# Optimization experiments

Hardware: AMD Instinct MI355X
Metric: run time of the kernel (lower is better)

## Reference

```python
import jax, jax.numpy as jnp
import numpy as np

N_Q, N_K = 4096, 32768
D_IN_Q, D_IN_V = 1024, 1024
D_QK, D_V = 512, 512
MASK_VAL = -1000.0


def setup_inputs() -> dict:
    key = jax.random.key(0)
    ks = jax.random.split(key, 9)
    X1 = jax.random.normal(ks[0], (N_Q, D_IN_Q), dtype=jnp.float32)
    X2 = jax.random.normal(ks[1], (N_K, D_IN_V), dtype=jnp.float32)
    row_map = jax.random.randint(ks[2], (N_K,), 0, N_Q, dtype=jnp.int32)
    # Linear params (stored as (in, out) for x @ W + b), xavier-ish scale
    def lin(k, din, dout):
        s = jnp.sqrt(6.0 / (din + dout)).astype(jnp.float32)
        return jax.random.uniform(k, (din, dout), jnp.float32, -s, s)
    Wq = lin(ks[3], D_IN_Q, D_QK); bq = jnp.zeros((D_QK,), jnp.float32)
    Wk = lin(ks[4], D_IN_V, D_QK); bk = jnp.zeros((D_QK,), jnp.float32)
    Wv = lin(ks[5], D_IN_V, D_V); bv = jnp.zeros((D_V,), jnp.float32)
    return {"X1": X1, "X2": X2, "Wq": Wq, "bq": bq, "Wk": Wk, "bk": bk,
            "Wv": Wv, "bv": bv, "row_map": row_map}


def reference(X1, X2, Wq, bq, Wk, bk, Wv, bv, row_map):
    n_q = X1.shape[0]
    n_k = X2.shape[0]
    Q = X1 @ Wq + bq                      # (n_q, d_qk)
    K = X2 @ Wk + bk                      # (n_k, d_qk)
    V = X2 @ Wv + bv                      # (n_k, d_v)
    scale = 1.0 / jnp.sqrt(jnp.float32(Q.shape[1]))
    S = (Q @ K.T) * scale                 # (n_q, n_k)
    cols = jnp.arange(n_k)
    # Keep only entries (row_map[j], j); everything else set to -1000 (as in torch)
    S_masked = jnp.full_like(S, MASK_VAL).at[row_map, cols].set(S[row_map, cols])
    W = jax.nn.softmax(S_masked, axis=1)  # (n_q, n_k)
    C = W @ V                             # (n_q, d_v)
    # Queries with no related keys get zero rows (torch skips them entirely)
    counts = jax.ops.segment_sum(jnp.ones((n_k,), jnp.float32), row_map,
                                 num_segments=n_q)
    return jnp.where(counts[:, None] > 0, C, jnp.zeros_like(C))
```

## Files before the change

kernel.cpp:

```cpp
#include <hip/hip_runtime.h>

typedef unsigned short bhalf;
typedef __bf16 bf16x8 __attribute__((ext_vector_type(8)));
typedef float f32x4 __attribute__((ext_vector_type(4)));

#define NQ 4096
#define NK 32768
#define DIN 1024
#define DQK 512
#define SCALE 0.044194173824159216f

__device__ __forceinline__ bhalf f2bf(float f) {
  union { float f; unsigned u; } c; c.f = f;
  unsigned u = c.u;
  return (bhalf)((u + 0x7fffu + ((u >> 16) & 1u)) >> 16);
}

__global__ void cvt_kernel(const float* __restrict__ in, bhalf* __restrict__ out, int n4) {
  const int i = blockIdx.x * 256 + threadIdx.x;
  float4 v = ((const float4*)in)[i];
  uint2 o;
  o.x = (unsigned)f2bf(v.x) | ((unsigned)f2bf(v.y) << 16);
  o.y = (unsigned)f2bf(v.z) | ((unsigned)f2bf(v.w) << 16);
  ((uint2*)out)[i] = o;
}

__global__ __launch_bounds__(256) void transpose_cvt_kernel(
    const float* __restrict__ in, bhalf* __restrict__ out) {
  const int Kdim = 1024, Ndim = 512;
  __shared__ float tile[32][33];
  const int tx = threadIdx.x, ty = threadIdx.y;
  const int x = blockIdx.x * 32 + tx;
#pragma unroll
  for (int yy = 0; yy < 32; yy += 8) {
    const int y = blockIdx.y * 32 + ty + yy;
    tile[ty + yy][tx] = in[(size_t)y * Ndim + x];
  }
  __syncthreads();
  const int k = blockIdx.y * 32 + tx;
#pragma unroll
  for (int yy = 0; yy < 32; yy += 8) {
    const int n = blockIdx.x * 32 + ty + yy;
    out[(size_t)n * Kdim + k] = f2bf(tile[tx][ty + yy]);
  }
}

__global__ __launch_bounds__(256) void gh_kernel(
    const float* __restrict__ Wk, const float* __restrict__ Wq,
    const float* __restrict__ bq, const float* __restrict__ bk,
    float* __restrict__ g_s, float* __restrict__ h, float* __restrict__ scal) {
  const int w = blockIdx.x * 4 + (threadIdx.x >> 6);
  const int lane = threadIdx.x & 63;
  if (w >= 2049) return;
  const float* row; const float* vec;
  if (w < 1024)      { row = Wk + (size_t)w * 512; vec = bq; }
  else if (w < 2048) { row = Wq + (size_t)(w - 1024) * 512; vec = bk; }
  else               { row = bq; vec = bk; }
  float s = 0.f;
#pragma unroll
  for (int t = 0; t < 2; t++) {
    float4 a = *(const float4*)(row + t * 256 + lane * 4);
    float4 b = *(const float4*)(vec + t * 256 + lane * 4);
    s += a.x * b.x + a.y * b.y + a.z * b.z + a.w * b.w;
  }
#pragma unroll
  for (int d = 32; d; d >>= 1) s += __shfl_xor(s, d);
  if (lane == 0) {
    if (w < 1024) g_s[w] = s * SCALE;
    else if (w < 2048) h[w - 1024] = s;
    else scal[0] = s;
  }
}

__global__ __launch_bounds__(256) void e_kernel(
    const float* __restrict__ X1, const float* __restrict__ h,
    const float* __restrict__ scal, float* __restrict__ ebuf) {
  const int i = blockIdx.x * 4 + (threadIdx.x >> 6);
  const int lane = threadIdx.x & 63;
  const float* xr = X1 + (size_t)i * 1024;
  float s = 0.f;
#pragma unroll
  for (int t = 0; t < 4; t++) {
    float4 a = *(const float4*)(xr + t * 256 + lane * 4);
    float4 b = *(const float4*)(h + t * 256 + lane * 4);
    s += a.x * b.x + a.y * b.y + a.z * b.z + a.w * b.w;
  }
#pragma unroll
  for (int d = 32; d; d >>= 1) s += __shfl_xor(s, d);
  if (lane == 0) ebuf[i] = (s + scal[0]) * SCALE;
}

template <int MODE>
__global__ __launch_bounds__(256) void gemm_core(
    const bhalf* __restrict__ A, const bhalf* __restrict__ Bt,
    const float* __restrict__ bias, const int* __restrict__ cnt,
    void* __restrict__ Cout, int M, int N, int K, int nnt) {
  __shared__ __align__(16) bhalf As[128 * 64];
  __shared__ __align__(16) bhalf Bs[128 * 64];
  const int bid = blockIdx.x;
  const int mt = bid / nnt, nt = bid % nnt;
  const int bmb = mt * 128, bnb = nt * 128;

  const int tid = threadIdx.x;
  const int lane = tid & 63;
  const int wv = tid >> 6;
  const int wm = (wv & 1) * 64;
  const int wn = (wv >> 1) * 64;
  const int quad = lane >> 4;
  const int l15 = lane & 15;

  f32x4 acc[4][4];
#pragma unroll
  for (int i = 0; i < 4; i++)
#pragma unroll
    for (int j = 0; j < 4; j++)
#pragma unroll
      for (int r = 0; r < 4; r++) acc[i][j][r] = 0.0f;

  const int srow = lane >> 3;
  const int scol = (lane & 7) ^ srow;

  for (int kb = 0; kb < K; kb += 64) {
#pragma unroll
    for (int r = 0; r < 4; r++) {
      const int chunk = wv * 4 + r;
      const int row = chunk * 8 + srow;
      const size_t goff = (size_t)kb + (size_t)scol * 8;
      __builtin_amdgcn_global_load_lds(
          (__attribute__((address_space(1))) unsigned int*)(A + (size_t)(bmb + row) * K + goff),
          (__attribute__((address_space(3))) unsigned int*)(As + chunk * 512), 16, 0, 0);
      __builtin_amdgcn_global_load_lds(
          (__attribute__((address_space(1))) unsigned int*)(Bt + (size_t)(bnb + row) * K + goff),
          (__attribute__((address_space(3))) unsigned int*)(Bs + chunk * 512), 16, 0, 0);
    }
    __syncthreads();
#pragma unroll
    for (int ks = 0; ks < 2; ks++) {
      const int su = ((ks * 4 + quad) ^ (lane & 7)) * 8;
      bf16x8 af[4], bfr[4];
#pragma unroll
      for (int i = 0; i < 4; i++) {
        af[i]  = *(const bf16x8*)(As + (wm + i * 16 + l15) * 64 + su);
        bfr[i] = *(const bf16x8*)(Bs + (wn + i * 16 + l15) * 64 + su);
      }
#pragma unroll
      for (int i = 0; i < 4; i++)
#pragma unroll
        for (int j = 0; j < 4; j++)
          acc[i][j] = __builtin_amdgcn_mfma_f32_16x16x32_bf16(af[i], bfr[j], acc[i][j], 0, 0, 0);
    }
    __syncthreads();
  }
#pragma unroll
  for (int j = 0; j < 4; j++) {
    const int col = bnb + wn + j * 16 + l15;
    const float bs = (MODE >= 1) ? bias[col] : 0.0f;
#pragma unroll
    for (int i = 0; i < 4; i++) {
#pragma unroll
      for (int r = 0; r < 4; r++) {
        const int row = bmb + wm + i * 16 + quad * 4 + r;
        const float v = acc[i][j][r];
        if (MODE == 0) {
          ((bhalf*)Cout)[(size_t)row * N + col] = f2bf(v * SCALE);
        } else if (MODE == 1) {
          ((float*)Cout)[(size_t)row * N + col] = v + bs;
        } else {
          ((float*)Cout)[(size_t)row * N + col] = (cnt[row] > 0) ? (v + bs) : 0.0f;
        }
      }
    }
  }
}

__global__ void hist_kernel(const int* __restrict__ rm, int* __restrict__ cnt) {
  const int j = blockIdx.x * 256 + threadIdx.x;
  atomicAdd(&cnt[rm[j]], 1);
}

__global__ __launch_bounds__(1024) void scan_kernel(const int* __restrict__ cnt,
                                                    int* __restrict__ off,
                                                    int* __restrict__ cur) {
  const int t = threadIdx.x;
  int4 v = ((const int4*)cnt)[t];
  const int sum = v.x + v.y + v.z + v.w;
  const int lane = t & 63, w = t >> 6;
  int x = sum;
#pragma unroll
  for (int d = 1; d < 64; d <<= 1) {
    int y = __shfl_up(x, d);
    if (lane >= d) x += y;
  }
  __shared__ int wsum[16];
  if (lane == 63) wsum[w] = x;
  __syncthreads();
  if (t == 0) {
    int a = 0;
    for (int i = 0; i < 16; i++) { int tv = wsum[i]; wsum[i] = a; a += tv; }
  }
  __syncthreads();
  const int excl = x - sum + wsum[w];
  int4 o; o.x = excl; o.y = o.x + v.x; o.z = o.y + v.y; o.w = o.z + v.z;
  ((int4*)off)[t] = o;
  ((int4*)cur)[t] = o;
}

__global__ void scatter_kernel(const int* __restrict__ rm, int* __restrict__ cur,
                               int* __restrict__ keylist) {
  const int j = blockIdx.x * 256 + threadIdx.x;
  const int p = atomicAdd(&cur[rm[j]], 1);
  keylist[p] = j;
}

__global__ __launch_bounds__(256) void scorewsum_kernel(
    const float* __restrict__ P, const float* __restrict__ X2,
    const float* __restrict__ ebuf, const int* __restrict__ off,
    const int* __restrict__ cnt, const int* __restrict__ keylist,
    bhalf* __restrict__ Ub) {
  __shared__ float wbuf[4][256];
  const int wv = threadIdx.x >> 6;
  const int i = blockIdx.x * 4 + wv;
  const int lane = threadIdx.x & 63;
  const int c = cnt[i], base = off[i];
  const float* Prow = P + (size_t)i * 1024;
  float4 p[4];
#pragma unroll
  for (int t = 0; t < 4; t++) p[t] = *(const float4*)(Prow + t * 256 + lane * 4);
  const float e_i = ebuf[i];
  float sumw = 0.f;
  for (int pp = 0; pp < c; pp++) {
    const int j = keylist[base + pp];
    const float* xr = X2 + (size_t)j * 1024;
    float s = 0.f;
#pragma unroll
    for (int t = 0; t < 4; t++) {
      float4 x = *(const float4*)(xr + t * 256 + lane * 4);
      s += p[t].x * x.x + p[t].y * x.y + p[t].z * x.z + p[t].w * x.w;
    }
#pragma unroll
    for (int d = 32; d; d >>= 1) s += __shfl_xor(s, d);
    const float w = __expf(s + e_i);
    sumw += w;
    if (lane == 0) wbuf[wv][pp] = w;
  }
  __syncthreads();
  float4 u[4] = {};
  for (int pp = 0; pp < c; pp++) {
    const int j = keylist[base + pp];
    const float w = wbuf[wv][pp];
    const float* xr = X2 + (size_t)j * 1024;
#pragma unroll
    for (int t = 0; t < 4; t++) {
      float4 x = *(const float4*)(xr + t * 256 + lane * 4);
      u[t].x += w * x.x; u[t].y += w * x.y; u[t].z += w * x.z; u[t].w += w * x.w;
    }
  }
  const float inv = (c > 0) ? 1.f / sumw : 0.f;
  bhalf* urow = Ub + (size_t)i * 1024;
#pragma unroll
  for (int t = 0; t < 4; t++) {
    uint2 o;
    o.x = (unsigned)f2bf(u[t].x * inv) | ((unsigned)f2bf(u[t].y * inv) << 16);
    o.y = (unsigned)f2bf(u[t].z * inv) | ((unsigned)f2bf(u[t].w * inv) << 16);
    *(uint2*)(urow + t * 256 + lane * 4) = o;
  }
}

extern "C" void kernel_launch(void* const* d_in, const int* in_sizes, int n_in,
                              void* d_out, int out_size, void* d_ws, size_t ws_size,
                              hipStream_t stream) {
  const float* X1 = (const float*)d_in[0];
  const float* X2 = (const float*)d_in[1];
  const float* Wq = (const float*)d_in[2];
  const float* bq = (const float*)d_in[3];
  const float* Wk = (const float*)d_in[4];
  const float* bk = (const float*)d_in[5];
  const float* Wv = (const float*)d_in[6];
  const float* bv = (const float*)d_in[7];
  const int* row_map = (const int*)d_in[8];
  float* out = (float*)d_out;

  char* p = (char*)d_ws;
  bhalf* X1b  = (bhalf*)p; p += (size_t)NQ * DIN * 2;
  bhalf* Wq_b = (bhalf*)p; p += (size_t)DIN * DQK * 2;
  bhalf* Wk_b = (bhalf*)p; p += (size_t)DIN * DQK * 2;
  bhalf* WvT  = (bhalf*)p; p += (size_t)DQK * DIN * 2;
  bhalf* Bt2  = (bhalf*)p; p += (size_t)DIN * DIN * 2;
  float* Pbuf = (float*)p; p += (size_t)NQ * DIN * 4;
  bhalf* Ub   = (bhalf*)p; p += (size_t)NQ * DIN * 2;
  float* g_s  = (float*)p; p += DIN * 4;
  float* h    = (float*)p; p += DIN * 4;
  float* ebuf = (float*)p; p += NQ * 4;
  float* scal = (float*)p; p += 256;
  int* cnt    = (int*)p;   p += NQ * 4;
  int* off    = (int*)p;   p += NQ * 4;
  int* cur    = (int*)p;   p += NQ * 4;
  int* keylist = (int*)p;  p += NK * 4;

  hipMemsetAsync(cnt, 0, (size_t)NQ * 4, stream);

  cvt_kernel<<<NQ * DIN / 4 / 256, 256, 0, stream>>>(X1, X1b, NQ * DIN / 4);
  cvt_kernel<<<DIN * DQK / 4 / 256, 256, 0, stream>>>(Wq, Wq_b, DIN * DQK / 4);
  cvt_kernel<<<DIN * DQK / 4 / 256, 256, 0, stream>>>(Wk, Wk_b, DIN * DQK / 4);
  transpose_cvt_kernel<<<dim3(16, 32), dim3(32, 8), 0, stream>>>(Wv, WvT);
  gh_kernel<<<513, 256, 0, stream>>>(Wk, Wq, bq, bk, g_s, h, scal);
  e_kernel<<<NQ / 4, 256, 0, stream>>>(X1, h, scal, ebuf);

  hist_kernel<<<NK / 256, 256, 0, stream>>>(row_map, cnt);
  scan_kernel<<<1, 1024, 0, stream>>>(cnt, off, cur);
  scatter_kernel<<<NK / 256, 256, 0, stream>>>(row_map, cur, keylist);

  gemm_core<0><<<64, 256, 0, stream>>>(Wk_b, Wq_b, nullptr, nullptr, Bt2, 1024, 1024, 512, 8);
  gemm_core<1><<<256, 256, 0, stream>>>(X1b, Bt2, g_s, nullptr, Pbuf, 4096, 1024, 1024, 8);

  scorewsum_kernel<<<NQ / 4, 256, 0, stream>>>(Pbuf, X2, ebuf, off, cnt, keylist, Ub);

  gemm_core<2><<<128, 256, 0, stream>>>(Ub, WvT, bv, cnt, out, 4096, 512, 1024, 4);
}
```

Measured before the change: 324.7 us.

## Fuse prep kernels, single-pass score/weighted-sum, and smaller M tiles for small GEMMs

Merges the three cvt launches, the Wv transpose, the gh reduction and the histogram into one block-indexed prep kernel to cut launch overhead. Moves the per-query e_i computation into the score kernel and merges its two passes over X2 into one. Each X2 row is now read once into registers and used for both the score and the weighted sum, removing the shared buffer and the barrier. Adds an MI template parameter so the Bt2 and output GEMMs use 64-row tiles and launch twice as many blocks, trading per-block reuse for better CU coverage.

```diff
diff --git a/kernel.cpp b/kernel.cpp
--- a/kernel.cpp
+++ b/kernel.cpp
@@ -10,108 +10,96 @@
 #define DQK 512
 #define SCALE 0.044194173824159216f
 
-__device__ __forceinline__ bhalf f2bf(float f) {
+__device__ __forceinline__ unsigned f2bf(float f) {
   union { float f; unsigned u; } c; c.f = f;
   unsigned u = c.u;
-  return (bhalf)((u + 0x7fffu + ((u >> 16) & 1u)) >> 16);
-}
-
-__global__ void cvt_kernel(const float* __restrict__ in, bhalf* __restrict__ out, int n4) {
-  const int i = blockIdx.x * 256 + threadIdx.x;
-  float4 v = ((const float4*)in)[i];
-  uint2 o;
-  o.x = (unsigned)f2bf(v.x) | ((unsigned)f2bf(v.y) << 16);
-  o.y = (unsigned)f2bf(v.z) | ((unsigned)f2bf(v.w) << 16);
-  ((uint2*)out)[i] = o;
-}
-
-__global__ __launch_bounds__(256) void transpose_cvt_kernel(
-    const float* __restrict__ in, bhalf* __restrict__ out) {
-  const int Kdim = 1024, Ndim = 512;
+  return (u + 0x7fffu + ((u >> 16) & 1u)) >> 16;
+}
+
+__global__ __launch_bounds__(256) void prep_kernel(
+    const float* __restrict__ X1, const float* __restrict__ Wq,
+    const float* __restrict__ Wk, const float* __restrict__ Wv,
+    const float* __restrict__ bq, const float* __restrict__ bk,
+    const int* __restrict__ rm,
+    bhalf* __restrict__ X1b, bhalf* __restrict__ Wq_b, bhalf* __restrict__ Wk_b,
+    bhalf* __restrict__ WvT, float* __restrict__ g_s, float* __restrict__ h,
+    float* __restrict__ scal, int* __restrict__ cnt) {
   __shared__ float tile[32][33];
-  const int tx = threadIdx.x, ty = threadIdx.y;
-  const int x = blockIdx.x * 32 + tx;
-#pragma unroll
-  for (int yy = 0; yy < 32; yy += 8) {
-    const int y = blockIdx.y * 32 + ty + yy;
-    tile[ty + yy][tx] = in[(size_t)y * Ndim + x];
-  }
-  __syncthreads();
-  const int k = blockIdx.y * 32 + tx;
-#pragma unroll
-  for (int yy = 0; yy < 32; yy += 8) {
-    const int n = blockIdx.x * 32 + ty + yy;
-    out[(size_t)n * Kdim + k] = f2bf(tile[tx][ty + yy]);
-  }
-}
-
-__global__ __launch_bounds__(256) void gh_kernel(
-    const float* __restrict__ Wk, const float* __restrict__ Wq,
-    const float* __restrict__ bq, const float* __restrict__ bk,
-    float* __restrict__ g_s, float* __restrict__ h, float* __restrict__ scal) {
-  const int w = blockIdx.x * 4 + (threadIdx.x >> 6);
-  const int lane = threadIdx.x & 63;
-  if (w >= 2049) return;
-  const float* row; const float* vec;
-  if (w < 1024)      { row = Wk + (size_t)w * 512; vec = bq; }
-  else if (w < 2048) { row = Wq + (size_t)(w - 1024) * 512; vec = bk; }
-  else               { row = bq; vec = bk; }
-  float s = 0.f;
-#pragma unroll
-  for (int t = 0; t < 2; t++) {
-    float4 a = *(const float4*)(row + t * 256 + lane * 4);
-    float4 b = *(const float4*)(vec + t * 256 + lane * 4);
-    s += a.x * b.x + a.y * b.y + a.z * b.z + a.w * b.w;
-  }
-#pragma unroll
-  for (int d = 32; d; d >>= 1) s += __shfl_xor(s, d);
-  if (lane == 0) {
-    if (w < 1024) g_s[w] = s * SCALE;
-    else if (w < 2048) h[w - 1024] = s;
-    else scal[0] = s;
-  }
-}
-
-__global__ __launch_bounds__(256) void e_kernel(
-    const float* __restrict__ X1, const float* __restrict__ h,
-    const float* __restrict__ scal, float* __restrict__ ebuf) {
-  const int i = blockIdx.x * 4 + (threadIdx.x >> 6);
-  const int lane = threadIdx.x & 63;
-  const float* xr = X1 + (size_t)i * 1024;
-  float s = 0.f;
-#pragma unroll
-  for (int t = 0; t < 4; t++) {
-    float4 a = *(const float4*)(xr + t * 256 + lane * 4);
-    float4 b = *(const float4*)(h + t * 256 + lane * 4);
-    s += a.x * b.x + a.y * b.y + a.z * b.z + a.w * b.w;
-  }
-#pragma unroll
-  for (int d = 32; d; d >>= 1) s += __shfl_xor(s, d);
-  if (lane == 0) ebuf[i] = (s + scal[0]) * SCALE;
-}
-
-template <int MODE>
+  const int b = blockIdx.x;
+  const int tid = threadIdx.x;
+  if (b < 5120) {
+    const float* in; bhalf* out; int idx;
+    if (b < 4096)      { in = X1; out = X1b; idx = b * 256 + tid; }
+    else if (b < 4608) { in = Wq; out = Wq_b; idx = (b - 4096) * 256 + tid; }
+    else               { in = Wk; out = Wk_b; idx = (b - 4608) * 256 + tid; }
+    float4 v = ((const float4*)in)[idx];
+    uint2 o;
+    o.x = f2bf(v.x) | (f2bf(v.y) << 16);
+    o.y = f2bf(v.z) | (f2bf(v.w) << 16);
+    ((uint2*)out)[idx] = o;
+  } else if (b < 5632) {
+    const int bb = b - 5120;
+    const int bx = bb & 15, by = bb >> 4;
+    const int tx = tid & 31, ty = tid >> 5;
+    const int x = bx * 32 + tx;
+#pragma unroll
+    for (int yy = 0; yy < 32; yy += 8)
+      tile[ty + yy][tx] = Wv[(size_t)(by * 32 + ty + yy) * 512 + x];
+    __syncthreads();
+    const int k = by * 32 + tx;
+#pragma unroll
+    for (int yy = 0; yy < 32; yy += 8)
+      WvT[(size_t)(bx * 32 + ty + yy) * 1024 + k] = (bhalf)f2bf(tile[tx][ty + yy]);
+  } else if (b < 6145) {
+    const int w = (b - 5632) * 4 + (tid >> 6);
+    const int lane = tid & 63;
+    if (w >= 2049) return;
+    const float* row; const float* vec;
+    if (w < 1024)      { row = Wk + (size_t)w * 512; vec = bq; }
+    else if (w < 2048) { row = Wq + (size_t)(w - 1024) * 512; vec = bk; }
+    else               { row = bq; vec = bk; }
+    float s = 0.f;
+#pragma unroll
+    for (int t = 0; t < 2; t++) {
+      float4 a = *(const float4*)(row + t * 256 + lane * 4);
+      float4 bb2 = *(const float4*)(vec + t * 256 + lane * 4);
+      s += a.x * bb2.x + a.y * bb2.y + a.z * bb2.z + a.w * bb2.w;
+    }
+#pragma unroll
+    for (int d = 32; d; d >>= 1) s += __shfl_xor(s, d);
+    if (lane == 0) {
+      if (w < 1024) g_s[w] = s * SCALE;
+      else if (w < 2048) h[w - 1024] = s;
+      else scal[0] = s;
+    }
+  } else {
+    const int j = (b - 6145) * 256 + tid;
+    atomicAdd(&cnt[rm[j]], 1);
+  }
+}
+
+template <int MODE, int MI>
 __global__ __launch_bounds__(256) void gemm_core(
     const bhalf* __restrict__ A, const bhalf* __restrict__ Bt,
     const float* __restrict__ bias, const int* __restrict__ cnt,
     void* __restrict__ Cout, int M, int N, int K, int nnt) {
-  __shared__ __align__(16) bhalf As[128 * 64];
+  __shared__ __align__(16) bhalf As[MI * 32 * 64];
   __shared__ __align__(16) bhalf Bs[128 * 64];
   const int bid = blockIdx.x;
   const int mt = bid / nnt, nt = bid % nnt;
-  const int bmb = mt * 128, bnb = nt * 128;
+  const int bmb = mt * (MI * 32), bnb = nt * 128;
 
   const int tid = threadIdx.x;
   const int lane = tid & 63;
   const int wv = tid >> 6;
-  const int wm = (wv & 1) * 64;
+  const int wm = (wv & 1) * (MI * 16);
   const int wn = (wv >> 1) * 64;
   const int quad = lane >> 4;
   const int l15 = lane & 15;
 
-  f32x4 acc[4][4];
-#pragma unroll
-  for (int i = 0; i < 4; i++)
+  f32x4 acc[MI][4];
+#pragma unroll
+  for (int i = 0; i < MI; i++)
 #pragma unroll
     for (int j = 0; j < 4; j++)
 #pragma unroll
@@ -121,14 +109,19 @@
   const int scol = (lane & 7) ^ srow;
 
   for (int kb = 0; kb < K; kb += 64) {
+    const size_t goff = (size_t)kb + (size_t)scol * 8;
+#pragma unroll
+    for (int r = 0; r < MI; r++) {
+      const int chunk = wv * MI + r;
+      const int row = chunk * 8 + srow;
+      __builtin_amdgcn_global_load_lds(
+          (__attribute__((address_space(1))) unsigned int*)(A + (size_t)(bmb + row) * K + goff),
+          (__attribute__((address_space(3))) unsigned int*)(As + chunk * 512), 16, 0, 0);
+    }
 #pragma unroll
     for (int r = 0; r < 4; r++) {
       const int chunk = wv * 4 + r;
       const int row = chunk * 8 + srow;
-      const size_t goff = (size_t)kb + (size_t)scol * 8;
-      __builtin_amdgcn_global_load_lds(
-          (__attribute__((address_space(1))) unsigned int*)(A + (size_t)(bmb + row) * K + goff),
-          (__attribute__((address_space(3))) unsigned int*)(As + chunk * 512), 16, 0, 0);
       __builtin_amdgcn_global_load_lds(
           (__attribute__((address_space(1))) unsigned int*)(Bt + (size_t)(bnb + row) * K + goff),
           (__attribute__((address_space(3))) unsigned int*)(Bs + chunk * 512), 16, 0, 0);
@@ -137,14 +130,15 @@
 #pragma unroll
     for (int ks = 0; ks < 2; ks++) {
       const int su = ((ks * 4 + quad) ^ (lane & 7)) * 8;
-      bf16x8 af[4], bfr[4];
-#pragma unroll
-      for (int i = 0; i < 4; i++) {
-        af[i]  = *(const bf16x8*)(As + (wm + i * 16 + l15) * 64 + su);
-        bfr[i] = *(const bf16x8*)(Bs + (wn + i * 16 + l15) * 64 + su);
-      }
-#pragma unroll
-      for (int i = 0; i < 4; i++)
+      bf16x8 af[MI], bfr[4];
+#pragma unroll
+      for (int i = 0; i < MI; i++)
+        af[i] = *(const bf16x8*)(As + (wm + i * 16 + l15) * 64 + su);
+#pragma unroll
+      for (int j = 0; j < 4; j++)
+        bfr[j] = *(const bf16x8*)(Bs + (wn + j * 16 + l15) * 64 + su);
+#pragma unroll
+      for (int i = 0; i < MI; i++)
 #pragma unroll
         for (int j = 0; j < 4; j++)
           acc[i][j] = __builtin_amdgcn_mfma_f32_16x16x32_bf16(af[i], bfr[j], acc[i][j], 0, 0, 0);
@@ -156,13 +150,13 @@
     const int col = bnb + wn + j * 16 + l15;
     const float bs = (MODE >= 1) ? bias[col] : 0.0f;
 #pragma unroll
-    for (int i = 0; i < 4; i++) {
+    for (int i = 0; i < MI; i++) {
 #pragma unroll
       for (int r = 0; r < 4; r++) {
         const int row = bmb + wm + i * 16 + quad * 4 + r;
         const float v = acc[i][j][r];
         if (MODE == 0) {
-          ((bhalf*)Cout)[(size_t)row * N + col] = f2bf(v * SCALE);
+          ((bhalf*)Cout)[(size_t)row * N + col] = (bhalf)f2bf(v * SCALE);
         } else if (MODE == 1) {
           ((float*)Cout)[(size_t)row * N + col] = v + bs;
         } else {
@@ -171,11 +165,6 @@
       }
     }
   }
-}
-
-__global__ void hist_kernel(const int* __restrict__ rm, int* __restrict__ cnt) {
-  const int j = blockIdx.x * 256 + threadIdx.x;
-  atomicAdd(&cnt[rm[j]], 1);
 }
 
 __global__ __launch_bounds__(1024) void scan_kernel(const int* __restrict__ cnt,
@@ -213,11 +202,11 @@
 }
 
 __global__ __launch_bounds__(256) void scorewsum_kernel(
-    const float* __restrict__ P, const float* __restrict__ X2,
-    const float* __restrict__ ebuf, const int* __restrict__ off,
+    const float* __restrict__ P, const float* __restrict__ X1,
+    const float* __restrict__ X2, const float* __restrict__ h,
+    const float* __restrict__ scal, const int* __restrict__ off,
     const int* __restrict__ cnt, const int* __restrict__ keylist,
     bhalf* __restrict__ Ub) {
-  __shared__ float wbuf[4][256];
   const int wv = threadIdx.x >> 6;
   const int i = blockIdx.x * 4 + wv;
   const int lane = threadIdx.x & 63;
@@ -226,33 +215,38 @@
   float4 p[4];
 #pragma unroll
   for (int t = 0; t < 4; t++) p[t] = *(const float4*)(Prow + t * 256 + lane * 4);
-  const float e_i = ebuf[i];
+  const float* x1r = X1 + (size_t)i * 1024;
+  float s0 = 0.f;
+#pragma unroll
+  for (int t = 0; t < 4; t++) {
+    float4 a = *(const float4*)(x1r + t * 256 + lane * 4);
+    float4 b = *(const float4*)(h + t * 256 + lane * 4);
+    s0 += a.x * b.x + a.y * b.y + a.z * b.z + a.w * b.w;
+  }
+#pragma unroll
+  for (int d = 32; d; d >>= 1) s0 += __shfl_xor(s0, d);
+  const float e_i = (s0 + scal[0]) * SCALE;
+
   float sumw = 0.f;
+  float4 u[4] = {};
   for (int pp = 0; pp < c; pp++) {
     const int j = keylist[base + pp];
     const float* xr = X2 + (size_t)j * 1024;
+    float4 x[4];
+#pragma unroll
+    for (int t = 0; t < 4; t++) x[t] = *(const float4*)(xr + t * 256 + lane * 4);
     float s = 0.f;
 #pragma unroll
-    for (int t = 0; t < 4; t++) {
-      float4 x = *(const float4*)(xr + t * 256 + lane * 4);
-      s += p[t].x * x.x + p[t].y * x.y + p[t].z * x.z + p[t].w * x.w;
-    }
+    for (int t = 0; t < 4; t++)
+      s += p[t].x * x[t].x + p[t].y * x[t].y + p[t].z * x[t].z + p[t].w * x[t].w;
 #pragma unroll
     for (int d = 32; d; d >>= 1) s += __shfl_xor(s, d);
     const float w = __expf(s + e_i);
     sumw += w;
-    if (lane == 0) wbuf[wv][pp] = w;
-  }
-  __syncthreads();
-  float4 u[4] = {};
-  for (int pp = 0; pp < c; pp++) {
-    const int j = keylist[base + pp];
-    const float w = wbuf[wv][pp];
-    const float* xr = X2 + (size_t)j * 1024;
 #pragma unroll
     for (int t = 0; t < 4; t++) {
-      float4 x = *(const float4*)(xr + t * 256 + lane * 4);
-      u[t].x += w * x.x; u[t].y += w * x.y; u[t].z += w * x.z; u[t].w += w * x.w;
+      u[t].x += w * x[t].x; u[t].y += w * x[t].y;
+      u[t].z += w * x[t].z; u[t].w += w * x[t].w;
     }
   }
   const float inv = (c > 0) ? 1.f / sumw : 0.f;
@@ -260,8 +254,8 @@
 #pragma unroll
   for (int t = 0; t < 4; t++) {
     uint2 o;
-    o.x = (unsigned)f2bf(u[t].x * inv) | ((unsigned)f2bf(u[t].y * inv) << 16);
-    o.y = (unsigned)f2bf(u[t].z * inv) | ((unsigned)f2bf(u[t].w * inv) << 16);
+    o.x = f2bf(u[t].x * inv) | (f2bf(u[t].y * inv) << 16);
+    o.y = f2bf(u[t].z * inv) | (f2bf(u[t].w * inv) << 16);
     *(uint2*)(urow + t * 256 + lane * 4) = o;
   }
 }
@@ -290,7 +284,6 @@
   bhalf* Ub   = (bhalf*)p; p += (size_t)NQ * DIN * 2;
   float* g_s  = (float*)p; p += DIN * 4;
   float* h    = (float*)p; p += DIN * 4;
-  float* ebuf = (float*)p; p += NQ * 4;
   float* scal = (float*)p; p += 256;
   int* cnt    = (int*)p;   p += NQ * 4;
   int* off    = (int*)p;   p += NQ * 4;
@@ -299,21 +292,15 @@
 
   hipMemsetAsync(cnt, 0, (size_t)NQ * 4, stream);
 
-  cvt_kernel<<<NQ * DIN / 4 / 256, 256, 0, stream>>>(X1, X1b, NQ * DIN / 4);
-  cvt_kernel<<<DIN * DQK / 4 / 256, 256, 0, stream>>>(Wq, Wq_b, DIN * DQK / 4);
-  cvt_kernel<<<DIN * DQK / 4 / 256, 256, 0, stream>>>(Wk, Wk_b, DIN * DQK / 4);
-  transpose_cvt_kernel<<<dim3(16, 32), dim3(32, 8), 0, stream>>>(Wv, WvT);
-  gh_kernel<<<513, 256, 0, stream>>>(Wk, Wq, bq, bk, g_s, h, scal);
-  e_kernel<<<NQ / 4, 256, 0, stream>>>(X1, h, scal, ebuf);
-
-  hist_kernel<<<NK / 256, 256, 0, stream>>>(row_map, cnt);
+  prep_kernel<<<6273, 256, 0, stream>>>(X1, Wq, Wk, Wv, bq, bk, row_map,
+                                        X1b, Wq_b, Wk_b, WvT, g_s, h, scal, cnt);
   scan_kernel<<<1, 1024, 0, stream>>>(cnt, off, cur);
   scatter_kernel<<<NK / 256, 256, 0, stream>>>(row_map, cur, keylist);
 
-  gemm_core<0><<<64, 256, 0, stream>>>(Wk_b, Wq_b, nullptr, nullptr, Bt2, 1024, 1024, 512, 8);
-  gemm_core<1><<<256, 256, 0, stream>>>(X1b, Bt2, g_s, nullptr, Pbuf, 4096, 1024, 1024, 8);
-
-  scorewsum_kernel<<<NQ / 4, 256, 0, stream>>>(Pbuf, X2, ebuf, off, cnt, keylist, Ub);
-
-  gemm_core<2><<<128, 256, 0, stream>>>(Ub, WvT, bv, cnt, out, 4096, 512, 1024, 4);
-}
+  gemm_core<0, 2><<<128, 256, 0, stream>>>(Wk_b, Wq_b, nullptr, nullptr, Bt2, 1024, 1024, 512, 8);
+  gemm_core<1, 4><<<256, 256, 0, stream>>>(X1b, Bt2, g_s, nullptr, Pbuf, 4096, 1024, 1024, 8);
+
+  scorewsum_kernel<<<NQ / 4, 256, 0, stream>>>(Pbuf, X1, X2, h, scal, off, cnt, keylist, Ub);
+
+  gemm_core<2, 2><<<256, 256, 0, stream>>>(Ub, WvT, bv, cnt, out, 4096, 512, 1024, 4);
+}
```

Result: faster. 297.2 us (-8.5%).
